# Performance work log

Hardware: AMD Instinct MI355X
Metric: run time of the kernel (lower is better)

Reference implementation:

```python
import math
import jax, jax.numpy as jnp
import numpy as np

# ---- static config ----
B, S, HID = 2, 8192, 1024
H, D = 8, 128                      # num_heads, head_dim = hidden // heads
CHUNK = 128                        # attention_chunk_size
PAST = 128 - 1                     # attention_context_left - 1
FUT = 128                          # attention_context_right
CTX = CHUNK + PAST + FUT           # 383
POS = CTX + 1                      # relative position table length (rel_shift pads to CTX+1)
CAP = 50.0                         # attention_logit_cap
Q_SCALE = D ** (-0.5) / math.log(2.0)
K_SCALE = math.log1p(math.e) / math.log(2.0)
NB = S // CHUNK                    # 64 blocks (S divisible by chunk -> no tail padding)


def setup_inputs() -> dict:
    key = jax.random.key(0)
    ks = jax.random.split(key, 8)
    s = 0.02
    return {
        "hidden_states": jax.random.normal(ks[0], (B, S, HID), jnp.float32),
        "position_embeddings": jax.random.normal(ks[1], (POS, HID), jnp.float32),
        "Wq": jax.random.normal(ks[2], (HID, H * D), jnp.float32) * s,
        "Wk": jax.random.normal(ks[3], (HID, H * D), jnp.float32) * s,
        "Wv": jax.random.normal(ks[4], (HID, H * D), jnp.float32) * s,
        "Wrel": jax.random.normal(ks[5], (HID, H * D), jnp.float32) * s,
        "Wpost": jax.random.normal(ks[6], (HID, HID), jnp.float32) * s,
        "per_dim_scale": jax.random.normal(ks[7], (D,), jnp.float32) * 0.1,
    }


def reference(hidden_states, position_embeddings, Wq, Wk, Wv, Wrel, Wpost, per_dim_scale):
    # projections (clipped-linear clamps are +/-inf -> no-ops); bias-free linears
    q = (hidden_states @ Wq).reshape(B, S, H, D)
    k = (hidden_states @ Wk).reshape(B, S, H, D)
    v = (hidden_states @ Wv).reshape(B, S, H, D)

    q = q * (Q_SCALE * jax.nn.softplus(per_dim_scale))  # per-dim scaling fused into q
    k = k * K_SCALE

    # _convert_to_block: [B, NB, CHUNK, H, D] (S % CHUNK == 0 -> no pad)
    qb = q.reshape(B, NB, CHUNK, H, D)

    # _extract_block_context: pad (PAST, FUT + CHUNK - 1) then unfold window=CTX step=CHUNK
    pad = ((0, 0), (PAST, FUT + CHUNK - 1), (0, 0), (0, 0))
    kp = jnp.pad(k, pad)
    vp = jnp.pad(v, pad)
    idx = jnp.arange(NB)[:, None] * CHUNK + jnp.arange(CTX)[None, :]  # [NB, CTX]
    kc = kp[:, idx]  # [B, NB, CTX, H, D]
    vc = vp[:, idx]  # [B, NB, CTX, H, D]

    # relative keys: [POS, H, D]
    rel_k = (position_embeddings @ Wrel).reshape(POS, H, D)

    # content scores: [B, H, NB, CHUNK, CTX]
    ac = jnp.einsum('bnchd,bnkhd->bhnck', qb, kc)
    # position scores before shift: [B, H, NB, CHUNK, POS]
    bd = jnp.einsum('bnchd,phd->bhncp', qb, rel_k)
    # Transformer-XL rel_shift (POS == CTX+1 so pad amount is zero)
    bd = bd.reshape(B, H, NB, CHUNK * POS)[..., : CHUNK * CTX]
    bd = bd.reshape(B, H, NB, CHUNK, CTX)

    # tanh soft-cap + softmax (no attention_mask)
    logits = jnp.tanh((ac + bd) / CAP) * CAP
    attn = jax.nn.softmax(logits, axis=-1)

    # weighted values -> [B, NB, CHUNK, H, D] -> [B, S, HID]
    out = jnp.einsum('bhnck,bnkhd->bnchd', attn, vc).reshape(B, S, H * D)
    return out @ Wpost
```

## Files before the change

### kernel.cpp

```cpp
#include <hip/hip_runtime.h>
#include <cmath>


using bf16x8 = __attribute__((ext_vector_type(8))) short;
using f32x4  = __attribute__((ext_vector_type(4))) float;
using s16x4  = __attribute__((ext_vector_type(4))) short;

__device__ __forceinline__ short f2bf(float f) {
  unsigned u = __float_as_uint(f);
  u = (u + 0x7FFF + ((u >> 16) & 1)) >> 16;
  return (short)u;
}
__device__ __forceinline__ float bf2f(unsigned short s) {
  return __uint_as_float(((unsigned)s) << 16);
}

__device__ __forceinline__ void gl16(void* lds, const void* gptr) {
  __builtin_amdgcn_global_load_lds(
      (const __attribute__((address_space(1))) unsigned int*)gptr,
      (__attribute__((address_space(3))) unsigned int*)lds, 16, 0, 0);
}

__global__ void cvt_bf16_k(const float* __restrict__ in, short* __restrict__ out, int n) {
  int i = (blockIdx.x * 256 + threadIdx.x) * 4;
  if (i + 3 < n) {
    float4 v = *(const float4*)&in[i];
    s16x4 o;
    o[0] = f2bf(v.x); o[1] = f2bf(v.y); o[2] = f2bf(v.z); o[3] = f2bf(v.w);
    *(s16x4*)&out[i] = o;
  }
}

__global__ void wtrans_k(const float* __restrict__ W, short* __restrict__ Wt) {
  __shared__ float T[64 * 65];
  const int tid = threadIdx.x;
  const int bx = blockIdx.x, by = blockIdx.y;
#pragma unroll
  for (int it = 0; it < 4; ++it) {
    int ci = it * 256 + tid;
    int k = ci >> 4, n4 = (ci & 15) * 4;
    float4 v = *(const float4*)&W[(size_t)(by * 64 + k) * 1024 + bx * 64 + n4];
    T[k * 65 + n4 + 0] = v.x;
    T[k * 65 + n4 + 1] = v.y;
    T[k * 65 + n4 + 2] = v.z;
    T[k * 65 + n4 + 3] = v.w;
  }
  __syncthreads();
#pragma unroll
  for (int it = 0; it < 2; ++it) {
    int co = it * 256 + tid;
    int nn = co >> 3, k8 = (co & 7) * 8;
    bf16x8 o;
#pragma unroll
    for (int jj = 0; jj < 8; ++jj) o[jj] = f2bf(T[(k8 + jj) * 65 + nn]);
    *(bf16x8*)&Wt[(size_t)(bx * 64 + nn) * 1024 + by * 64 + k8] = o;
  }
}

__global__ void qscale_k(const float* __restrict__ pds, float* __restrict__ qs, double qsb) {
  int d = threadIdx.x;
  double x = (double)pds[d];
  qs[d] = (float)(qsb * log1p(exp(x)));
}

__global__ void vpadzero_k(short* __restrict__ vpadT) {
  int row = blockIdx.x;
  int t = threadIdx.x;
  int key = (t < 127) ? t : (8192 + t);
  vpadT[(size_t)row * 8448 + key] = 0;
}

template <int MODE>
__global__ __launch_bounds__(256, 2)
void gemm_bt_k(const short* __restrict__ A, const short* __restrict__ Bt,
               short* __restrict__ outs, float* __restrict__ outf,
               const float* __restrict__ qsc, float kscale) {
  __shared__ __align__(16) short As[128 * 32];
  __shared__ __align__(16) short Bs[128 * 32];
  __shared__ __align__(16) short Tv[(MODE == 2) ? (128 * 136) : 16];

  const int tid = threadIdx.x;
  const int lane = tid & 63, wid = tid >> 6;
  const int q4 = lane >> 4, l16 = lane & 15;
  const int wr = wid >> 1, wc = wid & 1;
  const int m0 = blockIdx.x * 128, n0 = blockIdx.y * 128;

  const f32x4 z4 = {0.f, 0.f, 0.f, 0.f};
  f32x4 acc[4][4];
#pragma unroll
  for (int i = 0; i < 4; ++i)
#pragma unroll
    for (int j = 0; j < 4; ++j) acc[i][j] = z4;

  const int r0 = tid >> 2, s0_ = (tid & 3) * 8;

  for (int kk = 0; kk < 1024; kk += 32) {
    __syncthreads();
    gl16(&As[tid * 8],         A  + (size_t)(m0 + r0) * 1024 + kk + s0_);
    gl16(&Bs[tid * 8],         Bt + (size_t)(n0 + r0) * 1024 + kk + s0_);
    gl16(&As[(256 + tid) * 8], A  + (size_t)(m0 + 64 + r0) * 1024 + kk + s0_);
    gl16(&Bs[(256 + tid) * 8], Bt + (size_t)(n0 + 64 + r0) * 1024 + kk + s0_);
    __syncthreads();
    bf16x8 af[4], bfv[4];
#pragma unroll
    for (int i = 0; i < 4; ++i)
      af[i] = *(const bf16x8*)&As[(wr * 64 + i * 16 + l16) * 32 + q4 * 8];
#pragma unroll
    for (int j = 0; j < 4; ++j)
      bfv[j] = *(const bf16x8*)&Bs[(wc * 64 + j * 16 + l16) * 32 + q4 * 8];
#pragma unroll
    for (int i = 0; i < 4; ++i)
#pragma unroll
      for (int j = 0; j < 4; ++j)
        acc[i][j] = __builtin_amdgcn_mfma_f32_16x16x32_bf16(af[i], bfv[j], acc[i][j], 0, 0, 0);
  }

  float qsv[4];
  if (MODE == 0) {
#pragma unroll
    for (int j = 0; j < 4; ++j) qsv[j] = qsc[wc * 64 + j * 16 + l16];
  }

#pragma unroll
  for (int i = 0; i < 4; ++i) {
#pragma unroll
    for (int j = 0; j < 4; ++j) {
#pragma unroll
      for (int rg = 0; rg < 4; ++rg) {
        const int row = m0 + wr * 64 + i * 16 + q4 * 4 + rg;
        const int col = n0 + wc * 64 + j * 16 + l16;
        const float v = acc[i][j][rg];
        if (MODE == 0) {
          int b = row >> 13, s = row & 8191;
          int n = s >> 7, c = s & 127;
          int h = col >> 7, d = col & 127;
          outs[((size_t)(((b * 64 + n) * 8 + h) * 128 + c)) * 128 + d] = f2bf(v * qsv[j]);
        } else if (MODE == 1) {
          int b = row >> 13, s = row & 8191;
          int h = col >> 7, d = col & 127;
          outs[((size_t)(b * 8 + h) * 8448 + 127 + s) * 128 + d] = f2bf(v * kscale);
        } else if (MODE == 2) {
          int dl = wc * 64 + j * 16 + l16;
          int sl = wr * 64 + i * 16 + q4 * 4 + rg;
          Tv[dl * 136 + sl] = f2bf(v);
        } else if (MODE == 3) {
          int h = col >> 7, d = col & 127;
          outs[(size_t)(h * 384 + row) * 128 + d] = f2bf(v);
        } else {
          outf[(size_t)row * 1024 + col] = v;
        }
      }
    }
  }

  if (MODE == 2) {
    __syncthreads();
    const int b = m0 >> 13, ss = m0 & 8191, h = n0 >> 7;
#pragma unroll
    for (int it = 0; it < 8; ++it) {
      int co = it * 256 + tid;
      int d = co >> 4, s8 = (co & 15) * 8;
      *(bf16x8*)&outs[((size_t)(b * 8 + h) * 128 + d) * 8448 + 127 + ss + s8] =
          *(const bf16x8*)&Tv[d * 136 + s8];
    }
  }
}

__global__ __launch_bounds__(256, 2)
void bd_gemm_k(const short* __restrict__ qb_b, const short* __restrict__ relk,
               short* __restrict__ bds) {
  __shared__ __align__(16) short As[128 * 32];
  __shared__ __align__(16) short Bs[128 * 32];
  const int tid = threadIdx.x;
  const int lane = tid & 63, wid = tid >> 6;
  const int q4 = lane >> 4, l16 = lane & 15;
  const int wr = wid >> 1, wc = wid & 1;
  const int p0 = blockIdx.x * 128;
  const int nh = blockIdx.y;
  const int h = nh & 7;
  const short* A = qb_b + (size_t)nh * 16384;
  const short* Bt = relk + (size_t)h * (384 * 128);
  short* bdo = bds + (size_t)nh * 49152;

  const f32x4 z4 = {0.f, 0.f, 0.f, 0.f};
  f32x4 acc[4][4];
#pragma unroll
  for (int i = 0; i < 4; ++i)
#pragma unroll
    for (int j = 0; j < 4; ++j) acc[i][j] = z4;

  const int r0 = tid >> 2, s0_ = (tid & 3) * 8;
  for (int kk = 0; kk < 128; kk += 32) {
    __syncthreads();
    gl16(&As[tid * 8],         A  + (size_t)r0 * 128 + kk + s0_);
    gl16(&Bs[tid * 8],         Bt + (size_t)(p0 + r0) * 128 + kk + s0_);
    gl16(&As[(256 + tid) * 8], A  + (size_t)(64 + r0) * 128 + kk + s0_);
    gl16(&Bs[(256 + tid) * 8], Bt + (size_t)(p0 + 64 + r0) * 128 + kk + s0_);
    __syncthreads();
    bf16x8 af[4], bfv[4];
#pragma unroll
    for (int i = 0; i < 4; ++i)
      af[i] = *(const bf16x8*)&As[(wr * 64 + i * 16 + l16) * 32 + q4 * 8];
#pragma unroll
    for (int j = 0; j < 4; ++j)
      bfv[j] = *(const bf16x8*)&Bs[(wc * 64 + j * 16 + l16) * 32 + q4 * 8];
#pragma unroll
    for (int i = 0; i < 4; ++i)
#pragma unroll
      for (int j = 0; j < 4; ++j)
        acc[i][j] = __builtin_amdgcn_mfma_f32_16x16x32_bf16(af[i], bfv[j], acc[i][j], 0, 0, 0);
  }

#pragma unroll
  for (int i = 0; i < 4; ++i)
#pragma unroll
    for (int j = 0; j < 4; ++j)
#pragma unroll
      for (int rg = 0; rg < 4; ++rg) {
        int r = wr * 64 + i * 16 + q4 * 4 + rg;
        int p = p0 + wc * 64 + j * 16 + l16;
        int t = r + p;
        int c = (t < 383) ? r : (r + 1);
        int k = (t < 383) ? t : (t - 383);
        if (c < 128) {
          int tt = k >> 7, jj = (k >> 4) & 7, ll = k & 15;
          int wa = c >> 5, ia = (c >> 4) & 1, qa = (c >> 2) & 3, ra = c & 3;
          bdo[((((size_t)tt * 8 + jj) * 256) + wa * 64 + qa * 16 + ll) * 8 + ia * 4 + ra] =
              f2bf(acc[i][j][rg]);
        }
      }
}

__global__ __launch_bounds__(256, 2)
void attn_k(const short* __restrict__ qb_b, const short* __restrict__ kpad,
            const short* __restrict__ vpadT, const short* __restrict__ bds,
            short* __restrict__ attnout, int b) {
  __shared__ __align__(16) short Ks[4 * 128 * 32];
  __shared__ __align__(16) short Ps[2 * 128 * 40];

  const int tid = threadIdx.x;
  const int lane = tid & 63, wid = tid >> 6;
  const int q4 = lane >> 4, l16 = lane & 15;
  const int bx = blockIdx.x;
  const int n = bx >> 3, h = bx & 7;

  const short* qtile = qb_b + (size_t)bx * 16384;
  const short* kbase = kpad + ((size_t)(b * 8 + h) * 8448 + n * 128) * 128;
  const short* vtb = vpadT + (size_t)(b * 8 + h) * 128 * 8448 + n * 128;
  const short* bdb = bds + (size_t)bx * 49152;

#pragma unroll
  for (int it = 0; it < 8; ++it) {
    int ci = it * 256 + tid;
    int dc = ci >> 9, rr = (ci >> 2) & 127, sub = (ci & 3) * 8;
    gl16(&Ks[ci * 8], qtile + rr * 128 + dc * 32 + sub);
  }
  __syncthreads();
  bf16x8 qf[2][4];
#pragma unroll
  for (int i = 0; i < 2; ++i)
#pragma unroll
    for (int dc = 0; dc < 4; ++dc)
      qf[i][dc] = *(const bf16x8*)&Ks[dc * 4096 + (wid * 32 + i * 16 + l16) * 32 + q4 * 8];

  const f32x4 z4 = {0.f, 0.f, 0.f, 0.f};
  f32x4 acco[2][8];
#pragma unroll
  for (int i = 0; i < 2; ++i)
#pragma unroll
    for (int j = 0; j < 8; ++j) acco[i][j] = z4;
  float rsum[2][4] = {};

  for (int t = 0; t < 3; ++t) {
    __syncthreads();
#pragma unroll
    for (int it = 0; it < 8; ++it) {
      int ci = it * 256 + tid;
      int dc = ci >> 9, rr = (ci >> 2) & 127, sub = (ci & 3) * 8;
      gl16(&Ks[ci * 8], kbase + (size_t)(t * 128 + rr) * 128 + dc * 32 + sub);
    }

    bf16x8 bdv[8];
#pragma unroll
    for (int j = 0; j < 8; ++j)
      bdv[j] = *(const bf16x8*)&bdb[(((size_t)t * 8 + j) * 256 + wid * 64 + lane) * 8];

    __syncthreads();

    f32x4 accs[2][8];
#pragma unroll
    for (int i = 0; i < 2; ++i)
#pragma unroll
      for (int j = 0; j < 8; ++j) accs[i][j] = z4;
#pragma unroll
    for (int dc = 0; dc < 4; ++dc) {
      bf16x8 kf[8];
#pragma unroll
      for (int j = 0; j < 8; ++j)
        kf[j] = *(const bf16x8*)&Ks[dc * 4096 + (j * 16 + l16) * 32 + q4 * 8];
#pragma unroll
      for (int i = 0; i < 2; ++i)
#pragma unroll
        for (int j = 0; j < 8; ++j)
          accs[i][j] = __builtin_amdgcn_mfma_f32_16x16x32_bf16(qf[i][dc], kf[j], accs[i][j], 0, 0, 0);
    }

#pragma unroll
    for (int i = 0; i < 2; ++i) {
#pragma unroll
      for (int j = 0; j < 8; ++j) {
        const int kg = t * 128 + j * 16 + l16;
#pragma unroll
        for (int rg = 0; rg < 4; ++rg) {
          float sv = accs[i][j][rg] + bf2f((unsigned short)bdv[j][i * 4 + rg]);
          float tt = exp2f(sv * 0.057707801635558534f);
          float wgt = exp2f(-144.26950408889634f * __fdividef(1.0f, tt + 1.0f));
          wgt = (kg < 383) ? wgt : 0.0f;
          accs[i][j][rg] = wgt;
          rsum[i][rg] += wgt;
        }
      }
    }
    __syncthreads();

#pragma unroll
    for (int it = 0; it < 8; ++it) {
      int ci = it * 256 + tid;
      int kc = ci >> 9, dd = (ci >> 2) & 127, sub = (ci & 3) * 8;
      gl16(&Ks[ci * 8], vtb + (size_t)dd * 8448 + t * 128 + kc * 32 + sub);
    }
#pragma unroll
    for (int i = 0; i < 2; ++i)
#pragma unroll
      for (int j = 0; j < 4; ++j)
#pragma unroll
        for (int rg = 0; rg < 4; ++rg) {
          int c = wid * 32 + i * 16 + q4 * 4 + rg;
          int kl = j * 16 + l16;
          Ps[((kl >> 5) & 1) * 5120 + c * 40 + (kl & 31)] = f2bf(accs[i][j][rg]);
        }
    __syncthreads();
#pragma unroll
    for (int kc = 0; kc < 2; ++kc) {
      bf16x8 pf[2], vf[8];
#pragma unroll
      for (int i = 0; i < 2; ++i)
        pf[i] = *(const bf16x8*)&Ps[(kc & 1) * 5120 + (wid * 32 + i * 16 + l16) * 40 + q4 * 8];
#pragma unroll
      for (int j = 0; j < 8; ++j)
        vf[j] = *(const bf16x8*)&Ks[kc * 4096 + (j * 16 + l16) * 32 + q4 * 8];
#pragma unroll
      for (int i = 0; i < 2; ++i)
#pragma unroll
        for (int j = 0; j < 8; ++j)
          acco[i][j] = __builtin_amdgcn_mfma_f32_16x16x32_bf16(pf[i], vf[j], acco[i][j], 0, 0, 0);
    }
    __syncthreads();
#pragma unroll
    for (int i = 0; i < 2; ++i)
#pragma unroll
      for (int j = 4; j < 8; ++j)
#pragma unroll
        for (int rg = 0; rg < 4; ++rg) {
          int c = wid * 32 + i * 16 + q4 * 4 + rg;
          int kl = j * 16 + l16;
          Ps[((kl >> 5) & 1) * 5120 + c * 40 + (kl & 31)] = f2bf(accs[i][j][rg]);
        }
    __syncthreads();
#pragma unroll
    for (int kc = 2; kc < 4; ++kc) {
      bf16x8 pf[2], vf[8];
#pragma unroll
      for (int i = 0; i < 2; ++i)
        pf[i] = *(const bf16x8*)&Ps[(kc & 1) * 5120 + (wid * 32 + i * 16 + l16) * 40 + q4 * 8];
#pragma unroll
      for (int j = 0; j < 8; ++j)
        vf[j] = *(const bf16x8*)&Ks[kc * 4096 + (j * 16 + l16) * 32 + q4 * 8];
#pragma unroll
      for (int i = 0; i < 2; ++i)
#pragma unroll
        for (int j = 0; j < 8; ++j)
          acco[i][j] = __builtin_amdgcn_mfma_f32_16x16x32_bf16(pf[i], vf[j], acco[i][j], 0, 0, 0);
    }
  }

  float rinv[2][4];
#pragma unroll
  for (int i = 0; i < 2; ++i)
#pragma unroll
    for (int rg = 0; rg < 4; ++rg) {
      float rs = rsum[i][rg];
      rs += __shfl_xor(rs, 1);
      rs += __shfl_xor(rs, 2);
      rs += __shfl_xor(rs, 4);
      rs += __shfl_xor(rs, 8);
      rinv[i][rg] = __fdividef(1.0f, rs);
    }
#pragma unroll
  for (int i = 0; i < 2; ++i)
#pragma unroll
    for (int j = 0; j < 8; ++j)
#pragma unroll
      for (int rg = 0; rg < 4; ++rg) {
        int srow = n * 128 + wid * 32 + i * 16 + q4 * 4 + rg;
        int col = h * 128 + j * 16 + l16;
        attnout[((size_t)b * 8192 + srow) * 1024 + col] = f2bf(acco[i][j][rg] * rinv[i][rg]);
      }
}

extern "C" void kernel_launch(void* const* d_in, const int* in_sizes, int n_in,
                              void* d_out, int out_size, void* d_ws, size_t ws_size,
                              hipStream_t stream) {
  (void)in_sizes; (void)n_in; (void)out_size; (void)ws_size;
  const float* hs    = (const float*)d_in[0];
  const float* pemb  = (const float*)d_in[1];
  const float* Wq    = (const float*)d_in[2];
  const float* Wk    = (const float*)d_in[3];
  const float* Wv    = (const float*)d_in[4];
  const float* Wrel  = (const float*)d_in[5];
  const float* Wpost = (const float*)d_in[6];
  const float* pds   = (const float*)d_in[7];
  float* out = (float*)d_out;

  char* w = (char*)d_ws;
  auto alloc = [&](size_t bytes) -> char* {
    char* p = w; w += (bytes + 255) & ~(size_t)255; return p;
  };
  short* hs_bf   = (short*)alloc((size_t)16384 * 1024 * 2);
  short* pos_bf  = (short*)alloc((size_t)384 * 1024 * 2);
  short* Wq_t    = (short*)alloc((size_t)1024 * 1024 * 2);
  short* Wk_t    = (short*)alloc((size_t)1024 * 1024 * 2);
  short* Wv_t    = (short*)alloc((size_t)1024 * 1024 * 2);
  short* Wrel_t  = (short*)alloc((size_t)1024 * 1024 * 2);
  short* Wpost_t = (short*)alloc((size_t)1024 * 1024 * 2);
  float* qsc     = (float*)alloc(512);
  short* q_bf    = (short*)alloc((size_t)2 * 64 * 8 * 128 * 128 * 2);
  short* kpad    = (short*)alloc((size_t)2 * 8 * 8448 * 128 * 2);
  short* vpadT   = (short*)alloc((size_t)2 * 8 * 128 * 8448 * 2);
  short* relk    = (short*)alloc((size_t)8 * 384 * 128 * 2);
  short* bds     = (short*)alloc((size_t)64 * 8 * 128 * 384 * 2);
  short* attnout = hs_bf;

  const float kscale = (float)(log1p(exp(1.0)) / log(2.0));
  const double qsb = (1.0 / sqrt(128.0)) / log(2.0);

  cvt_bf16_k<<<16384, 256, 0, stream>>>(hs, hs_bf, 16384 * 1024);
  cvt_bf16_k<<<384, 256, 0, stream>>>(pemb, pos_bf, 384 * 1024);
  dim3 tg(16, 16);
  wtrans_k<<<tg, 256, 0, stream>>>(Wq, Wq_t);
  wtrans_k<<<tg, 256, 0, stream>>>(Wk, Wk_t);
  wtrans_k<<<tg, 256, 0, stream>>>(Wv, Wv_t);
  wtrans_k<<<tg, 256, 0, stream>>>(Wrel, Wrel_t);
  wtrans_k<<<tg, 256, 0, stream>>>(Wpost, Wpost_t);
  qscale_k<<<1, 128, 0, stream>>>(pds, qsc, qsb);
  hipMemsetAsync(kpad, 0, (size_t)2 * 8 * 8448 * 128 * 2, stream);
  vpadzero_k<<<2048, 256, 0, stream>>>(vpadT);

  dim3 g128(128, 8);
  gemm_bt_k<0><<<g128, 256, 0, stream>>>(hs_bf, Wq_t, q_bf, nullptr, qsc, 0.f);
  gemm_bt_k<1><<<g128, 256, 0, stream>>>(hs_bf, Wk_t, kpad, nullptr, qsc, kscale);
  gemm_bt_k<2><<<g128, 256, 0, stream>>>(hs_bf, Wv_t, vpadT, nullptr, qsc, 0.f);
  gemm_bt_k<3><<<dim3(3, 8), 256, 0, stream>>>(pos_bf, Wrel_t, relk, nullptr, qsc, 0.f);

  for (int b = 0; b < 2; ++b) {
    const short* qb_b = q_bf + (size_t)b * 64 * 8 * 128 * 128;
    bd_gemm_k<<<dim3(3, 512), 256, 0, stream>>>(qb_b, relk, bds);
    attn_k<<<512, 256, 0, stream>>>(qb_b, kpad, vpadT, bds, attnout, b);
  }

  gemm_bt_k<4><<<g128, 256, 0, stream>>>(attnout, Wpost_t, nullptr, out, qsc, 0.f);
}
```

Before: 573.7 us.

## Fuse QKV GEMMs into one XCD-swizzled launch and single-pass P staging

Replaces three separate Q/K/V projection launches with one 3072-block kernel that picks the weight matrix and output layout per block. It assumes Wq_t, Wk_t and Wv_t sit contiguously in memory. Block indices are remapped so each XCD works on a contiguous set of row tiles, for both the QKV GEMM and the output projection, which now runs at 3 blocks per CU. In attention, the whole 128x128 probability tile is staged to LDS at once instead of in two halves, which removes two barriers per iteration but uses more LDS.

Result: faster. 557.3 us (-2.9%).

```diff
diff --git a/kernel.cpp b/kernel.cpp
--- a/kernel.cpp
+++ b/kernel.cpp
@@ -70,14 +70,164 @@
   vpadT[(size_t)row * 8448 + key] = 0;
 }
 
-template <int MODE>
-__global__ __launch_bounds__(256, 2)
-void gemm_bt_k(const short* __restrict__ A, const short* __restrict__ Bt,
-               short* __restrict__ outs, float* __restrict__ outf,
-               const float* __restrict__ qsc, float kscale) {
+__global__ __launch_bounds__(256, 3)
+void qkv_fused_k(const short* __restrict__ A, const short* __restrict__ Bt3,
+                 short* __restrict__ q_bf, short* __restrict__ kpad,
+                 short* __restrict__ vpadT,
+                 const float* __restrict__ qsc, float kscale) {
   __shared__ __align__(16) short As[128 * 32];
   __shared__ __align__(16) short Bs[128 * 32];
-  __shared__ __align__(16) short Tv[(MODE == 2) ? (128 * 136) : 16];
+  __shared__ __align__(16) short Tv[128 * 136];
+
+  const int tid = threadIdx.x;
+  const int lane = tid & 63, wid = tid >> 6;
+  const int q4 = lane >> 4, l16 = lane & 15;
+  const int wr = wid >> 1, wc = wid & 1;
+
+  const int id = blockIdx.x;
+  const int xcd = id & 7, local = id >> 3;
+  const int mm = local / 24, nn = local - mm * 24;
+  const int m0 = (xcd * 16 + mm) * 128;
+  const int w = nn >> 3, nc = nn & 7;
+  const short* Bt = Bt3 + ((size_t)w * 1024 + nc * 128) * 1024;
+
+  const f32x4 z4 = {0.f, 0.f, 0.f, 0.f};
+  f32x4 acc[4][4];
+#pragma unroll
+  for (int i = 0; i < 4; ++i)
+#pragma unroll
+    for (int j = 0; j < 4; ++j) acc[i][j] = z4;
+
+  const int r0 = tid >> 2, s0_ = (tid & 3) * 8;
+
+  for (int kk = 0; kk < 1024; kk += 32) {
+    __syncthreads();
+    gl16(&As[tid * 8],         A  + (size_t)(m0 + r0) * 1024 + kk + s0_);
+    gl16(&Bs[tid * 8],         Bt + (size_t)r0 * 1024 + kk + s0_);
+    gl16(&As[(256 + tid) * 8], A  + (size_t)(m0 + 64 + r0) * 1024 + kk + s0_);
+    gl16(&Bs[(256 + tid) * 8], Bt + (size_t)(64 + r0) * 1024 + kk + s0_);
+    __syncthreads();
+    bf16x8 af[4], bfv[4];
+#pragma unroll
+    for (int i = 0; i < 4; ++i)
+      af[i] = *(const bf16x8*)&As[(wr * 64 + i * 16 + l16) * 32 + q4 * 8];
+#pragma unroll
+    for (int j = 0; j < 4; ++j)
+      bfv[j] = *(const bf16x8*)&Bs[(wc * 64 + j * 16 + l16) * 32 + q4 * 8];
+#pragma unroll
+    for (int i = 0; i < 4; ++i)
+#pragma unroll
+      for (int j = 0; j < 4; ++j)
+        acc[i][j] = __builtin_amdgcn_mfma_f32_16x16x32_bf16(af[i], bfv[j], acc[i][j], 0, 0, 0);
+  }
+
+  float qsv[4];
+  if (w == 0) {
+#pragma unroll
+    for (int j = 0; j < 4; ++j) qsv[j] = qsc[wc * 64 + j * 16 + l16];
+  }
+
+#pragma unroll
+  for (int i = 0; i < 4; ++i) {
+#pragma unroll
+    for (int j = 0; j < 4; ++j) {
+#pragma unroll
+      for (int rg = 0; rg < 4; ++rg) {
+        const int row = m0 + wr * 64 + i * 16 + q4 * 4 + rg;
+        const int d = wc * 64 + j * 16 + l16;
+        const int h = nc;
+        const float v = acc[i][j][rg];
+        if (w == 0) {
+          int b = row >> 13, s = row & 8191;
+          int n = s >> 7, c = s & 127;
+          q_bf[((size_t)(((b * 64 + n) * 8 + h) * 128 + c)) * 128 + d] = f2bf(v * qsv[j]);
+        } else if (w == 1) {
+          int b = row >> 13, s = row & 8191;
+          kpad[((size_t)(b * 8 + h) * 8448 + 127 + s) * 128 + d] = f2bf(v * kscale);
+        } else {
+          int sl = wr * 64 + i * 16 + q4 * 4 + rg;
+          Tv[d * 136 + sl] = f2bf(v);
+        }
+      }
+    }
+  }
+
+  if (w == 2) {
+    __syncthreads();
+    const int b = m0 >> 13, ss = m0 & 8191, h = nc;
+#pragma unroll
+    for (int it = 0; it < 8; ++it) {
+      int co = it * 256 + tid;
+      int d = co >> 4, s8 = (co & 15) * 8;
+      *(bf16x8*)&vpadT[((size_t)(b * 8 + h) * 128 + d) * 8448 + 127 + ss + s8] =
+          *(const bf16x8*)&Tv[d * 136 + s8];
+    }
+  }
+}
+
+__global__ __launch_bounds__(256, 3)
+void post_gemm_k(const short* __restrict__ A, const short* __restrict__ Bt,
+                 float* __restrict__ outf) {
+  __shared__ __align__(16) short As[128 * 32];
+  __shared__ __align__(16) short Bs[128 * 32];
+
+  const int tid = threadIdx.x;
+  const int lane = tid & 63, wid = tid >> 6;
+  const int q4 = lane >> 4, l16 = lane & 15;
+  const int wr = wid >> 1, wc = wid & 1;
+
+  const int id = blockIdx.x;
+  const int xcd = id & 7, local = id >> 3;
+  const int mm = local >> 3, nn = local & 7;
+  const int m0 = (xcd * 16 + mm) * 128, n0 = nn * 128;
+
+  const f32x4 z4 = {0.f, 0.f, 0.f, 0.f};
+  f32x4 acc[4][4];
+#pragma unroll
+  for (int i = 0; i < 4; ++i)
+#pragma unroll
+    for (int j = 0; j < 4; ++j) acc[i][j] = z4;
+
+  const int r0 = tid >> 2, s0_ = (tid & 3) * 8;
+
+  for (int kk = 0; kk < 1024; kk += 32) {
+    __syncthreads();
+    gl16(&As[tid * 8],         A  + (size_t)(m0 + r0) * 1024 + kk + s0_);
+    gl16(&Bs[tid * 8],         Bt + (size_t)(n0 + r0) * 1024 + kk + s0_);
+    gl16(&As[(256 + tid) * 8], A  + (size_t)(m0 + 64 + r0) * 1024 + kk + s0_);
+    gl16(&Bs[(256 + tid) * 8], Bt + (size_t)(n0 + 64 + r0) * 1024 + kk + s0_);
+    __syncthreads();
+    bf16x8 af[4], bfv[4];
+#pragma unroll
+    for (int i = 0; i < 4; ++i)
+      af[i] = *(const bf16x8*)&As[(wr * 64 + i * 16 + l16) * 32 + q4 * 8];
+#pragma unroll
+    for (int j = 0; j < 4; ++j)
+      bfv[j] = *(const bf16x8*)&Bs[(wc * 64 + j * 16 + l16) * 32 + q4 * 8];
+#pragma unroll
+    for (int i = 0; i < 4; ++i)
+#pragma unroll
+      for (int j = 0; j < 4; ++j)
+        acc[i][j] = __builtin_amdgcn_mfma_f32_16x16x32_bf16(af[i], bfv[j], acc[i][j], 0, 0, 0);
+  }
+
+#pragma unroll
+  for (int i = 0; i < 4; ++i)
+#pragma unroll
+    for (int j = 0; j < 4; ++j)
+#pragma unroll
+      for (int rg = 0; rg < 4; ++rg) {
+        const int row = m0 + wr * 64 + i * 16 + q4 * 4 + rg;
+        const int col = n0 + wc * 64 + j * 16 + l16;
+        outf[(size_t)row * 1024 + col] = acc[i][j][rg];
+      }
+}
+
+__global__ __launch_bounds__(256, 2)
+void rel_gemm_k(const short* __restrict__ A, const short* __restrict__ Bt,
+                short* __restrict__ relk) {
+  __shared__ __align__(16) short As[128 * 32];
+  __shared__ __align__(16) short Bs[128 * 32];
 
   const int tid = threadIdx.x;
   const int lane = tid & 63, wid = tid >> 6;
@@ -93,7 +243,6 @@
     for (int j = 0; j < 4; ++j) acc[i][j] = z4;
 
   const int r0 = tid >> 2, s0_ = (tid & 3) * 8;
-
   for (int kk = 0; kk < 1024; kk += 32) {
     __syncthreads();
     gl16(&As[tid * 8],         A  + (size_t)(m0 + r0) * 1024 + kk + s0_);
@@ -115,55 +264,17 @@
         acc[i][j] = __builtin_amdgcn_mfma_f32_16x16x32_bf16(af[i], bfv[j], acc[i][j], 0, 0, 0);
   }
 
-  float qsv[4];
-  if (MODE == 0) {
-#pragma unroll
-    for (int j = 0; j < 4; ++j) qsv[j] = qsc[wc * 64 + j * 16 + l16];
-  }
-
-#pragma unroll
-  for (int i = 0; i < 4; ++i) {
-#pragma unroll
-    for (int j = 0; j < 4; ++j) {
+#pragma unroll
+  for (int i = 0; i < 4; ++i)
+#pragma unroll
+    for (int j = 0; j < 4; ++j)
 #pragma unroll
       for (int rg = 0; rg < 4; ++rg) {
         const int row = m0 + wr * 64 + i * 16 + q4 * 4 + rg;
         const int col = n0 + wc * 64 + j * 16 + l16;
-        const float v = acc[i][j][rg];
-        if (MODE == 0) {
-          int b = row >> 13, s = row & 8191;
-          int n = s >> 7, c = s & 127;
-          int h = col >> 7, d = col & 127;
-          outs[((size_t)(((b * 64 + n) * 8 + h) * 128 + c)) * 128 + d] = f2bf(v * qsv[j]);
-        } else if (MODE == 1) {
-          int b = row >> 13, s = row & 8191;
-          int h = col >> 7, d = col & 127;
-          outs[((size_t)(b * 8 + h) * 8448 + 127 + s) * 128 + d] = f2bf(v * kscale);
-        } else if (MODE == 2) {
-          int dl = wc * 64 + j * 16 + l16;
-          int sl = wr * 64 + i * 16 + q4 * 4 + rg;
-          Tv[dl * 136 + sl] = f2bf(v);
-        } else if (MODE == 3) {
-          int h = col >> 7, d = col & 127;
-          outs[(size_t)(h * 384 + row) * 128 + d] = f2bf(v);
-        } else {
-          outf[(size_t)row * 1024 + col] = v;
-        }
+        int h = col >> 7, d = col & 127;
+        relk[(size_t)(h * 384 + row) * 128 + d] = f2bf(acc[i][j][rg]);
       }
-    }
-  }
-
-  if (MODE == 2) {
-    __syncthreads();
-    const int b = m0 >> 13, ss = m0 & 8191, h = n0 >> 7;
-#pragma unroll
-    for (int it = 0; it < 8; ++it) {
-      int co = it * 256 + tid;
-      int d = co >> 4, s8 = (co & 15) * 8;
-      *(bf16x8*)&outs[((size_t)(b * 8 + h) * 128 + d) * 8448 + 127 + ss + s8] =
-          *(const bf16x8*)&Tv[d * 136 + s8];
-    }
-  }
 }
 
 __global__ __launch_bounds__(256, 2)
@@ -236,7 +347,7 @@
             const short* __restrict__ vpadT, const short* __restrict__ bds,
             short* __restrict__ attnout, int b) {
   __shared__ __align__(16) short Ks[4 * 128 * 32];
-  __shared__ __align__(16) short Ps[2 * 128 * 40];
+  __shared__ __align__(16) short Ps[128 * 136];
 
   const int tid = threadIdx.x;
   const int lane = tid & 63, wid = tid >> 6;
@@ -332,47 +443,21 @@
 #pragma unroll
     for (int i = 0; i < 2; ++i)
 #pragma unroll
-      for (int j = 0; j < 4; ++j)
+      for (int j = 0; j < 8; ++j)
 #pragma unroll
         for (int rg = 0; rg < 4; ++rg) {
           int c = wid * 32 + i * 16 + q4 * 4 + rg;
           int kl = j * 16 + l16;
-          Ps[((kl >> 5) & 1) * 5120 + c * 40 + (kl & 31)] = f2bf(accs[i][j][rg]);
+          Ps[c * 136 + kl] = f2bf(accs[i][j][rg]);
         }
     __syncthreads();
-#pragma unroll
-    for (int kc = 0; kc < 2; ++kc) {
+
+#pragma unroll
+    for (int kc = 0; kc < 4; ++kc) {
       bf16x8 pf[2], vf[8];
 #pragma unroll
       for (int i = 0; i < 2; ++i)
-        pf[i] = *(const bf16x8*)&Ps[(kc & 1) * 5120 + (wid * 32 + i * 16 + l16) * 40 + q4 * 8];
-#pragma unroll
-      for (int j = 0; j < 8; ++j)
-        vf[j] = *(const bf16x8*)&Ks[kc * 4096 + (j * 16 + l16) * 32 + q4 * 8];
-#pragma unroll
-      for (int i = 0; i < 2; ++i)
-#pragma unroll
-        for (int j = 0; j < 8; ++j)
-          acco[i][j] = __builtin_amdgcn_mfma_f32_16x16x32_bf16(pf[i], vf[j], acco[i][j], 0, 0, 0);
-    }
-    __syncthreads();
-#pragma unroll
-    for (int i = 0; i < 2; ++i)
-#pragma unroll
-      for (int j = 4; j < 8; ++j)
-#pragma unroll
-        for (int rg = 0; rg < 4; ++rg) {
-          int c = wid * 32 + i * 16 + q4 * 4 + rg;
-          int kl = j * 16 + l16;
-          Ps[((kl >> 5) & 1) * 5120 + c * 40 + (kl & 31)] = f2bf(accs[i][j][rg]);
-        }
-    __syncthreads();
-#pragma unroll
-    for (int kc = 2; kc < 4; ++kc) {
-      bf16x8 pf[2], vf[8];
-#pragma unroll
-      for (int i = 0; i < 2; ++i)
-        pf[i] = *(const bf16x8*)&Ps[(kc & 1) * 5120 + (wid * 32 + i * 16 + l16) * 40 + q4 * 8];
+        pf[i] = *(const bf16x8*)&Ps[(wid * 32 + i * 16 + l16) * 136 + kc * 32 + q4 * 8];
 #pragma unroll
       for (int j = 0; j < 8; ++j)
         vf[j] = *(const bf16x8*)&Ks[kc * 4096 + (j * 16 + l16) * 32 + q4 * 8];
@@ -456,11 +541,8 @@
   hipMemsetAsync(kpad, 0, (size_t)2 * 8 * 8448 * 128 * 2, stream);
   vpadzero_k<<<2048, 256, 0, stream>>>(vpadT);
 
-  dim3 g128(128, 8);
-  gemm_bt_k<0><<<g128, 256, 0, stream>>>(hs_bf, Wq_t, q_bf, nullptr, qsc, 0.f);
-  gemm_bt_k<1><<<g128, 256, 0, stream>>>(hs_bf, Wk_t, kpad, nullptr, qsc, kscale);
-  gemm_bt_k<2><<<g128, 256, 0, stream>>>(hs_bf, Wv_t, vpadT, nullptr, qsc, 0.f);
-  gemm_bt_k<3><<<dim3(3, 8), 256, 0, stream>>>(pos_bf, Wrel_t, relk, nullptr, qsc, 0.f);
+  qkv_fused_k<<<3072, 256, 0, stream>>>(hs_bf, Wq_t, q_bf, kpad, vpadT, qsc, kscale);
+  rel_gemm_k<<<dim3(3, 8), 256, 0, stream>>>(pos_bf, Wrel_t, relk);
 
   for (int b = 0; b < 2; ++b) {
     const short* qb_b = q_bf + (size_t)b * 64 * 8 * 128 * 128;
@@ -468,5 +550,5 @@
     attn_k<<<512, 256, 0, stream>>>(qb_b, kpad, vpadT, bds, attnout, b);
   }
 
-  gemm_bt_k<4><<<g128, 256, 0, stream>>>(attnout, Wpost_t, nullptr, out, qsc, 0.f);
-}
+  post_gemm_k<<<1024, 256, 0, stream>>>(attnout, Wpost_t, out);
+}
```
